# Kernel tuning notes

Hardware: AMD Instinct MI355X
Metric: run time of the kernel (lower is better)

## Reference

```python
import jax, jax.numpy as jnp
import numpy as np

B, FIN, H, W = 16, 256, 32, 32
NH, FH = 8, 64
CIN = FIN + 2  # fin + 2 coordinate-grid pos channels
COUT = NH * FH


def setup_inputs() -> dict:
    key = jax.random.key(0)
    ks = jax.random.split(key, 9)
    s = 1.0 / np.sqrt(CIN)
    so = 1.0 / np.sqrt(COUT)
    return {
        "x": jax.random.normal(ks[0], (B, FIN, H, W), dtype=jnp.float32),
        "wq": jax.random.uniform(ks[1], (COUT, CIN), jnp.float32, -s, s),
        "bq": jax.random.uniform(ks[2], (COUT,), jnp.float32, -s, s),
        "wk": jax.random.uniform(ks[3], (COUT, CIN), jnp.float32, -s, s),
        "bk": jax.random.uniform(ks[4], (COUT,), jnp.float32, -s, s),
        "wv": jax.random.uniform(ks[5], (COUT, CIN), jnp.float32, -s, s),
        "bv": jax.random.uniform(ks[6], (COUT,), jnp.float32, -s, s),
        "wo": jax.random.uniform(ks[7], (FIN, COUT), jnp.float32, -so, so),
        "bo": jax.random.uniform(ks[8], (FIN,), jnp.float32, -so, so),
    }


def reference(x, wq, bq, wk, bk, wv, bv, wo, bo):
    b, c, h, w = x.shape
    n = h * w
    # PosEncoding: concat one linspace(-1,1) coordinate channel per spatial dim
    gy, gx = jnp.meshgrid(jnp.linspace(-1.0, 1.0, h), jnp.linspace(-1.0, 1.0, w), indexing="ij")
    pos = jnp.broadcast_to(jnp.stack([gy, gx])[None], (b, 2, h, w)).astype(x.dtype)
    t = jnp.concatenate([x, pos], axis=1).reshape(b, c + 2, n)  # [B, C+2, N]
    # 1x1 convs are per-token GEMMs
    q = (jnp.einsum("oc,bcn->bon", wq, t) + bq[:, None]).reshape(b, NH, FH, n)
    k = (jnp.einsum("oc,bcn->bon", wk, t) + bk[:, None]).reshape(b, NH, FH, n)
    v = (jnp.einsum("oc,bcn->bon", wv, t) + bv[:, None]).reshape(b, NH, FH, n)
    temp = FH ** 0.5
    attn = jax.nn.softmax(jnp.einsum("bhdn,bhdm->bhnm", q, k) / temp, axis=-1)
    o = jnp.einsum("bhnm,bhdm->bhdn", attn, v).reshape(b, NH * FH, n)
    o = jnp.einsum("oc,bcn->bon", wo, o) + bo[:, None]
    return x + o.reshape(b, c, h, w)
```

## Files before the change

### kernel.cpp

```cpp
#include <hip/hip_runtime.h>


typedef unsigned short u16;
typedef unsigned int   u32;
typedef __attribute__((ext_vector_type(8))) short  short8;
typedef __attribute__((ext_vector_type(4))) float  float4_;

#define MFMA16(a, b, c) __builtin_amdgcn_mfma_f32_16x16x32_bf16(a, b, c, 0, 0, 0)

__device__ __forceinline__ float bf2f(u16 u) {
    union { u32 i; float f; } v; v.i = ((u32)u) << 16; return v.f;
}
__device__ __forceinline__ u16 f2bf(float f) {
    union { float f; u32 i; } v; v.f = f;
    u32 r = v.i + 0x7FFFu + ((v.i >> 16) & 1u);
    return (u16)(r >> 16);
}
__device__ __forceinline__ u16 f2bf_fast(float f) {
    union { float f; u32 i; } v; v.f = f;
    return (u16)((v.i + 0x8000u) >> 16);
}

__global__ __launch_bounds__(256) void prep(
    const float* __restrict__ wq, const float* __restrict__ wk,
    const float* __restrict__ wv, const float* __restrict__ x,
    u16* __restrict__ wb, u16* __restrict__ xT)
{
    __shared__ float Lt[64][65];
    const int bid = blockIdx.x;
    const int tid = threadIdx.x;
    if (bid < 512) {
        int i = bid * 256 + tid;
        int o = i >> 8, c = i & 255;
        size_t si = (size_t)o * 258 + c;
        wb[i]          = f2bf(wq[si]);
        wb[131072 + i] = f2bf(wk[si]);
        wb[262144 + i] = f2bf(wv[si]);
    } else {
        int r = bid - 512;
        int n0 = (r & 15) * 64, c0 = ((r >> 4) & 3) * 64, b = r >> 6;
#pragma unroll
        for (int p = 0; p < 4; ++p) {
            int c = p * 16 + (tid >> 4);
            int nn = (tid & 15) * 4;
            float4 v = *(const float4*)&x[((size_t)(b * 256) + c0 + c) * 1024 + n0 + nn];
            Lt[c][nn + 0] = v.x; Lt[c][nn + 1] = v.y;
            Lt[c][nn + 2] = v.z; Lt[c][nn + 3] = v.w;
        }
        __syncthreads();
#pragma unroll
        for (int p = 0; p < 4; ++p) {
            int n = p * 16 + (tid >> 4);
            int cc = (tid & 15) * 4;
            ushort4 st;
            st.x = f2bf(Lt[cc + 0][n]); st.y = f2bf(Lt[cc + 1][n]);
            st.z = f2bf(Lt[cc + 2][n]); st.w = f2bf(Lt[cc + 3][n]);
            *(ushort4*)&xT[((size_t)(b << 10) + n0 + n) * 256 + c0 + cc] = st;
        }
    }
}

__global__ __launch_bounds__(256) void qkv_mfma(
    const u16* __restrict__ xT, const u16* __restrict__ wb,
    const float* __restrict__ wq, const float* __restrict__ wk,
    const float* __restrict__ wv,
    const float* __restrict__ bq, const float* __restrict__ bk,
    const float* __restrict__ bv,
    u16* __restrict__ qkvbuf)
{
    __shared__ u16 Wl[128][40];
    __shared__ u16 Tl[128][40];
    const int tid = threadIdx.x;
    const int lane = tid & 63, w = tid >> 6;
    const int quad = lane >> 4, m15 = lane & 15;
    const int n0 = blockIdx.x * 128, mt = blockIdx.y, b = blockIdx.z;
    const int mat = mt >> 2;
    const int m0 = mt * 128;
    const float* worig = (mat == 0) ? wq : ((mat == 1) ? wk : wv);
    const float* bias  = (mat == 0) ? bq : ((mat == 1) ? bk : bv);
    const float oscale = (mat == 1) ? 0.125f : 1.0f;
    u16* outbuf = qkvbuf + (size_t)mat * 8388608;

    float4_ acc[2][8];
#pragma unroll
    for (int s = 0; s < 2; ++s)
#pragma unroll
        for (int t = 0; t < 8; ++t) acc[s][t] = (float4_){0, 0, 0, 0};

    const int row = tid >> 2, col8 = (tid & 3) * 8;

    for (int cc0 = 0; cc0 < 256; cc0 += 32) {
        __syncthreads();
#pragma unroll
        for (int rr = 0; rr < 128; rr += 64) {
            *(short8*)&Wl[row + rr][col8] =
                *(const short8*)(wb + (size_t)(m0 + row + rr) * 256 + cc0 + col8);
            *(short8*)&Tl[row + rr][col8] =
                *(const short8*)(xT + ((size_t)(b << 10) + n0 + row + rr) * 256 + cc0 + col8);
        }
        __syncthreads();
        short8 af[2];
#pragma unroll
        for (int s = 0; s < 2; ++s)
            af[s] = *(const short8*)&Wl[w * 32 + s * 16 + m15][quad * 8];
#pragma unroll
        for (int t = 0; t < 8; ++t) {
            short8 bf = *(const short8*)&Tl[t * 16 + m15][quad * 8];
#pragma unroll
            for (int s = 0; s < 2; ++s)
                acc[s][t] = MFMA16(af[s], bf, acc[s][t]);
        }
    }

#pragma unroll
    for (int s = 0; s < 2; ++s) {
        float wg[4], wx[4], bi[4];
#pragma unroll
        for (int r = 0; r < 4; ++r) {
            int om = (mt & 3) * 128 + w * 32 + s * 16 + quad * 4 + r;
            wg[r] = worig[(size_t)om * 258 + 256];
            wx[r] = worig[(size_t)om * 258 + 257];
            bi[r] = bias[om];
        }
        const int h = (mt & 3) * 2 + ((w * 32 + s * 16) >> 6);
        const int dbase = ((w * 32 + s * 16) & 63) + quad * 4;
#pragma unroll
        for (int t = 0; t < 8; ++t) {
            int n = n0 + t * 16 + m15;
            float gy = -1.0f + 2.0f * (float)(n >> 5) / 31.0f;
            float gx = -1.0f + 2.0f * (float)(n & 31) / 31.0f;
            float v[4];
#pragma unroll
            for (int r = 0; r < 4; ++r)
                v[r] = (acc[s][t][r] + wg[r] * gy + wx[r] * gx + bi[r]) * oscale;
            if (mat != 2) {
                ushort4 st;
                st.x = f2bf(v[0]); st.y = f2bf(v[1]);
                st.z = f2bf(v[2]); st.w = f2bf(v[3]);
                *(ushort4*)&outbuf[((size_t)(b * 8 + h) * 1024 + n) * 64 + dbase] = st;
            } else {
#pragma unroll
                for (int r = 0; r < 4; ++r)
                    outbuf[((size_t)(b * 8 + h) * 64 + dbase + r) * 1024 + n] = f2bf(v[r]);
            }
        }
    }
}

__global__ __launch_bounds__(256) void attn_mfma(
    u16* __restrict__ qbuf, const u16* __restrict__ kbuf,
    const u16* __restrict__ vbuf)
{
    __shared__ u16 Kl[64 * 64];
    __shared__ u16 Vl[64 * 64];
    __shared__ u16 Pl[4][32][72];

    const int tid = threadIdx.x;
    const int lane = tid & 63, w = tid >> 6;
    const int quad = lane >> 4, m15 = lane & 15;
    const int bh = blockIdx.x;
    const int q0 = blockIdx.y * 128;
    u16* qb = qbuf + (size_t)bh * 65536;
    const u16* kb = kbuf + (size_t)bh * 65536;
    const u16* vb = vbuf + (size_t)bh * 65536;

    short8 qf[2][2];
#pragma unroll
    for (int s = 0; s < 2; ++s) {
        const u16* qr = qb + (size_t)(q0 + w * 32 + s * 16 + m15) * 64 + quad * 8;
        qf[s][0] = *(const short8*)qr;
        qf[s][1] = *(const short8*)(qr + 32);
    }

    float4_ O[2][4];
    float lp[2][4];
#pragma unroll
    for (int s = 0; s < 2; ++s)
#pragma unroll
        for (int t = 0; t < 4; ++t) { O[s][t] = (float4_){0,0,0,0}; lp[s][t] = 0.0f; }

    const int row = tid >> 3, c8 = (tid & 7) * 8;
    const int stsw = c8 ^ ((row & 7) << 3);
    const int rdsw = (m15 & 7) << 3;

    for (int kt0 = 0; kt0 < 1024; kt0 += 64) {
        __syncthreads();
#pragma unroll
        for (int rr = 0; rr < 64; rr += 32) {
            *(short8*)&Kl[(row + rr) * 64 + stsw] =
                *(const short8*)(kb + (size_t)(kt0 + row + rr) * 64 + c8);
            *(short8*)&Vl[(row + rr) * 64 + stsw] =
                *(const short8*)(vb + (size_t)(row + rr) * 1024 + kt0 + c8);
        }
        __syncthreads();

        float4_ S[2][4];
#pragma unroll
        for (int s = 0; s < 2; ++s)
#pragma unroll
            for (int t = 0; t < 4; ++t) S[s][t] = (float4_){0, 0, 0, 0};
#pragma unroll
        for (int c = 0; c < 2; ++c) {
            short8 bk[4];
#pragma unroll
            for (int t = 0; t < 4; ++t)
                bk[t] = *(const short8*)&Kl[(t * 16 + m15) * 64 +
                                            ((c * 32 + quad * 8) ^ rdsw)];
            __builtin_amdgcn_s_setprio(1);
#pragma unroll
            for (int s = 0; s < 2; ++s)
#pragma unroll
                for (int t = 0; t < 4; ++t)
                    S[s][t] = MFMA16(qf[s][c], bk[t], S[s][t]);
            __builtin_amdgcn_s_setprio(0);
        }

#pragma unroll
        for (int s = 0; s < 2; ++s)
#pragma unroll
            for (int r = 0; r < 4; ++r) {
                float p0 = __expf(S[s][0][r]);
                float p1 = __expf(S[s][1][r]);
                float p2 = __expf(S[s][2][r]);
                float p3 = __expf(S[s][3][r]);
                u16* pr = &Pl[w][s * 16 + quad * 4 + r][m15];
                pr[0]  = f2bf_fast(p0);
                pr[16] = f2bf_fast(p1);
                pr[32] = f2bf_fast(p2);
                pr[48] = f2bf_fast(p3);
                lp[s][r] += (p0 + p1) + (p2 + p3);
            }

#pragma unroll
        for (int c = 0; c < 2; ++c) {
            short8 av[4];
#pragma unroll
            for (int dt = 0; dt < 4; ++dt)
                av[dt] = *(const short8*)&Vl[(dt * 16 + m15) * 64 +
                                             ((c * 32 + quad * 8) ^ rdsw)];
#pragma unroll
            for (int s = 0; s < 2; ++s) {
                short8 bp = *(const short8*)&Pl[w][s * 16 + m15][c * 32 + quad * 8];
                __builtin_amdgcn_s_setprio(1);
#pragma unroll
                for (int dt = 0; dt < 4; ++dt)
                    O[s][dt] = MFMA16(av[dt], bp, O[s][dt]);
                __builtin_amdgcn_s_setprio(0);
            }
        }
    }

#pragma unroll
    for (int s = 0; s < 2; ++s)
#pragma unroll
        for (int r = 0; r < 4; ++r) {
            float v = lp[s][r];
            v += __shfl_xor(v, 1);
            v += __shfl_xor(v, 2);
            v += __shfl_xor(v, 4);
            v += __shfl_xor(v, 8);
            lp[s][r] = v;
        }

#pragma unroll
    for (int s = 0; s < 2; ++s) {
        int src = (m15 >> 2) * 16;
        float a0 = __shfl(lp[s][0], src);
        float a1 = __shfl(lp[s][1], src);
        float a2 = __shfl(lp[s][2], src);
        float a3 = __shfl(lp[s][3], src);
        int rr2 = m15 & 3;
        float lq = (rr2 & 2) ? ((rr2 & 1) ? a3 : a2) : ((rr2 & 1) ? a1 : a0);
        float linv = 1.0f / lq;
        int n = q0 + w * 32 + s * 16 + m15;
#pragma unroll
        for (int dt = 0; dt < 4; ++dt) {
            ushort4 st;
            st.x = f2bf(O[s][dt][0] * linv);
            st.y = f2bf(O[s][dt][1] * linv);
            st.z = f2bf(O[s][dt][2] * linv);
            st.w = f2bf(O[s][dt][3] * linv);
            *(ushort4*)&qb[(size_t)n * 64 + dt * 16 + quad * 4] = st;
        }
    }
}

__global__ __launch_bounds__(256) void proj_mfma(
    const u16* __restrict__ ao, const float* __restrict__ wo,
    const float* __restrict__ bo, const float* __restrict__ x,
    float* __restrict__ out)
{
    __shared__ u16 Wl[64][72];
    __shared__ u16 Tl[64][72];
    const int tid = threadIdx.x;
    const int lane = tid & 63, w = tid >> 6;
    const int quad = lane >> 4, m15 = lane & 15;
    const int n0 = blockIdx.x * 64, f0 = blockIdx.y * 64, b = blockIdx.z;

    float4_ acc[4] = {{0,0,0,0},{0,0,0,0},{0,0,0,0},{0,0,0,0}};
    const int row = tid >> 3, c8 = (tid & 7) * 8;

    for (int cc0 = 0; cc0 < 512; cc0 += 64) {
        __syncthreads();
        const int h = cc0 >> 6;
#pragma unroll
        for (int rr = 0; rr < 64; rr += 32) {
            const float* wsrc = wo + (size_t)(f0 + row + rr) * 512 + cc0 + c8;
            float4 v0 = *(const float4*)wsrc;
            float4 v1 = *(const float4*)(wsrc + 4);
            ushort4 s0, s1;
            s0.x = f2bf(v0.x); s0.y = f2bf(v0.y); s0.z = f2bf(v0.z); s0.w = f2bf(v0.w);
            s1.x = f2bf(v1.x); s1.y = f2bf(v1.y); s1.z = f2bf(v1.z); s1.w = f2bf(v1.w);
            *(ushort4*)&Wl[row + rr][c8]     = s0;
            *(ushort4*)&Wl[row + rr][c8 + 4] = s1;
            *(short8*)&Tl[row + rr][c8] =
                *(const short8*)(ao + ((size_t)((b << 3) + h) * 1024 + n0 + row + rr) * 64 + c8);
        }
        __syncthreads();
#pragma unroll
        for (int c = 0; c < 2; ++c) {
            short8 af = *(const short8*)&Wl[w * 16 + m15][c * 32 + quad * 8];
#pragma unroll
            for (int t = 0; t < 4; ++t) {
                short8 bf = *(const short8*)&Tl[t * 16 + m15][c * 32 + quad * 8];
                acc[t] = MFMA16(af, bf, acc[t]);
            }
        }
    }

    float bi[4];
#pragma unroll
    for (int r = 0; r < 4; ++r) bi[r] = bo[f0 + w * 16 + quad * 4 + r];
#pragma unroll
    for (int t = 0; t < 4; ++t) {
        int n = n0 + t * 16 + m15;
#pragma unroll
        for (int r = 0; r < 4; ++r) {
            int f = f0 + w * 16 + quad * 4 + r;
            size_t idx = ((size_t)(b * 256) + f) * 1024 + n;
            out[idx] = acc[t][r] + bi[r] + x[idx];
        }
    }
}

extern "C" void kernel_launch(void* const* d_in, const int* in_sizes, int n_in,
                              void* d_out, int out_size, void* d_ws, size_t ws_size,
                              hipStream_t stream) {
    const float* x  = (const float*)d_in[0];
    const float* wq = (const float*)d_in[1];
    const float* bq = (const float*)d_in[2];
    const float* wk = (const float*)d_in[3];
    const float* bk = (const float*)d_in[4];
    const float* wv = (const float*)d_in[5];
    const float* bv = (const float*)d_in[6];
    const float* wo = (const float*)d_in[7];
    const float* bo = (const float*)d_in[8];

    u16* qkvbuf = (u16*)d_ws;
    u16* region = qkvbuf + 3 * 8388608;
    u16* xT = region;
    u16* wb = region + 4194304;

    prep<<<1536, 256, 0, stream>>>(wq, wk, wv, x, wb, xT);

    qkv_mfma<<<dim3(8, 12, 16), 256, 0, stream>>>(
        xT, wb, wq, wk, wv, bq, bk, bv, qkvbuf);

    attn_mfma<<<dim3(128, 8), 256, 0, stream>>>(
        qkvbuf, qkvbuf + 8388608, qkvbuf + 16777216);

    proj_mfma<<<dim3(16, 4, 16), 256, 0, stream>>>(qkvbuf, wo, bo, x, (float*)d_out);
}
```

Measured before the change: 202.0 us.

## Split attention work over 8 waves with 16 query rows each

```diff
diff --git a/kernel.cpp b/kernel.cpp
--- a/kernel.cpp
+++ b/kernel.cpp
@@ -147,13 +147,13 @@
     }
 }
 
-__global__ __launch_bounds__(256) void attn_mfma(
+__global__ __launch_bounds__(512, 8) void attn_mfma(
     u16* __restrict__ qbuf, const u16* __restrict__ kbuf,
     const u16* __restrict__ vbuf)
 {
     __shared__ u16 Kl[64 * 64];
     __shared__ u16 Vl[64 * 64];
-    __shared__ u16 Pl[4][32][72];
+    __shared__ u16 Pl[8][16][72];
 
     const int tid = threadIdx.x;
     const int lane = tid & 63, w = tid >> 6;
@@ -164,20 +164,17 @@
     const u16* kb = kbuf + (size_t)bh * 65536;
     const u16* vb = vbuf + (size_t)bh * 65536;
 
-    short8 qf[2][2];
-#pragma unroll
-    for (int s = 0; s < 2; ++s) {
-        const u16* qr = qb + (size_t)(q0 + w * 32 + s * 16 + m15) * 64 + quad * 8;
-        qf[s][0] = *(const short8*)qr;
-        qf[s][1] = *(const short8*)(qr + 32);
-    }
-
-    float4_ O[2][4];
-    float lp[2][4];
-#pragma unroll
-    for (int s = 0; s < 2; ++s)
-#pragma unroll
-        for (int t = 0; t < 4; ++t) { O[s][t] = (float4_){0,0,0,0}; lp[s][t] = 0.0f; }
+    short8 qf[2];
+    {
+        const u16* qr = qb + (size_t)(q0 + w * 16 + m15) * 64 + quad * 8;
+        qf[0] = *(const short8*)qr;
+        qf[1] = *(const short8*)(qr + 32);
+    }
+
+    float4_ O[4];
+    float lp[4];
+#pragma unroll
+    for (int t = 0; t < 4; ++t) { O[t] = (float4_){0,0,0,0}; lp[t] = 0.0f; }
 
     const int row = tid >> 3, c8 = (tid & 7) * 8;
     const int stsw = c8 ^ ((row & 7) << 3);
@@ -185,20 +182,15 @@
 
     for (int kt0 = 0; kt0 < 1024; kt0 += 64) {
         __syncthreads();
-#pragma unroll
-        for (int rr = 0; rr < 64; rr += 32) {
-            *(short8*)&Kl[(row + rr) * 64 + stsw] =
-                *(const short8*)(kb + (size_t)(kt0 + row + rr) * 64 + c8);
-            *(short8*)&Vl[(row + rr) * 64 + stsw] =
-                *(const short8*)(vb + (size_t)(row + rr) * 1024 + kt0 + c8);
-        }
-        __syncthreads();
-
-        float4_ S[2][4];
-#pragma unroll
-        for (int s = 0; s < 2; ++s)
-#pragma unroll
-            for (int t = 0; t < 4; ++t) S[s][t] = (float4_){0, 0, 0, 0};
+        *(short8*)&Kl[row * 64 + stsw] =
+            *(const short8*)(kb + (size_t)(kt0 + row) * 64 + c8);
+        *(short8*)&Vl[row * 64 + stsw] =
+            *(const short8*)(vb + (size_t)row * 1024 + kt0 + c8);
+        __syncthreads();
+
+        float4_ S[4];
+#pragma unroll
+        for (int t = 0; t < 4; ++t) S[t] = (float4_){0, 0, 0, 0};
 #pragma unroll
         for (int c = 0; c < 2; ++c) {
             short8 bk[4];
@@ -208,78 +200,68 @@
                                             ((c * 32 + quad * 8) ^ rdsw)];
             __builtin_amdgcn_s_setprio(1);
 #pragma unroll
-            for (int s = 0; s < 2; ++s)
-#pragma unroll
-                for (int t = 0; t < 4; ++t)
-                    S[s][t] = MFMA16(qf[s][c], bk[t], S[s][t]);
+            for (int t = 0; t < 4; ++t)
+                S[t] = MFMA16(qf[c], bk[t], S[t]);
             __builtin_amdgcn_s_setprio(0);
         }
 
 #pragma unroll
-        for (int s = 0; s < 2; ++s)
-#pragma unroll
-            for (int r = 0; r < 4; ++r) {
-                float p0 = __expf(S[s][0][r]);
-                float p1 = __expf(S[s][1][r]);
-                float p2 = __expf(S[s][2][r]);
-                float p3 = __expf(S[s][3][r]);
-                u16* pr = &Pl[w][s * 16 + quad * 4 + r][m15];
-                pr[0]  = f2bf_fast(p0);
-                pr[16] = f2bf_fast(p1);
-                pr[32] = f2bf_fast(p2);
-                pr[48] = f2bf_fast(p3);
-                lp[s][r] += (p0 + p1) + (p2 + p3);
-            }
+        for (int r = 0; r < 4; ++r) {
+            float p0 = __expf(S[0][r]);
+            float p1 = __expf(S[1][r]);
+            float p2 = __expf(S[2][r]);
+            float p3 = __expf(S[3][r]);
+            u16* pr = &Pl[w][quad * 4 + r][m15];
+            pr[0]  = f2bf_fast(p0);
+            pr[16] = f2bf_fast(p1);
+            pr[32] = f2bf_fast(p2);
+            pr[48] = f2bf_fast(p3);
+            lp[r] += (p0 + p1) + (p2 + p3);
+        }
 
 #pragma unroll
         for (int c = 0; c < 2; ++c) {
+            short8 bp = *(const short8*)&Pl[w][m15][c * 32 + quad * 8];
             short8 av[4];
 #pragma unroll
             for (int dt = 0; dt < 4; ++dt)
                 av[dt] = *(const short8*)&Vl[(dt * 16 + m15) * 64 +
                                              ((c * 32 + quad * 8) ^ rdsw)];
-#pragma unroll
-            for (int s = 0; s < 2; ++s) {
-                short8 bp = *(const short8*)&Pl[w][s * 16 + m15][c * 32 + quad * 8];
-                __builtin_amdgcn_s_setprio(1);
-#pragma unroll
-                for (int dt = 0; dt < 4; ++dt)
-                    O[s][dt] = MFMA16(av[dt], bp, O[s][dt]);
-                __builtin_amdgcn_s_setprio(0);
-            }
-        }
-    }
-
-#pragma unroll
-    for (int s = 0; s < 2; ++s)
-#pragma unroll
-        for (int r = 0; r < 4; ++r) {
-            float v = lp[s][r];
-            v += __shfl_xor(v, 1);
-            v += __shfl_xor(v, 2);
-            v += __shfl_xor(v, 4);
-            v += __shfl_xor(v, 8);
-            lp[s][r] = v;
-        }
-
-#pragma unroll
-    for (int s = 0; s < 2; ++s) {
+            __builtin_amdgcn_s_setprio(1);
+#pragma unroll
+            for (int dt = 0; dt < 4; ++dt)
+                O[dt] = MFMA16(av[dt], bp, O[dt]);
+            __builtin_amdgcn_s_setprio(0);
+        }
+    }
+
+#pragma unroll
+    for (int r = 0; r < 4; ++r) {
+        float v = lp[r];
+        v += __shfl_xor(v, 1);
+        v += __shfl_xor(v, 2);
+        v += __shfl_xor(v, 4);
+        v += __shfl_xor(v, 8);
+        lp[r] = v;
+    }
+
+    {
         int src = (m15 >> 2) * 16;
-        float a0 = __shfl(lp[s][0], src);
-        float a1 = __shfl(lp[s][1], src);
-        float a2 = __shfl(lp[s][2], src);
-        float a3 = __shfl(lp[s][3], src);
+        float a0 = __shfl(lp[0], src);
+        float a1 = __shfl(lp[1], src);
+        float a2 = __shfl(lp[2], src);
+        float a3 = __shfl(lp[3], src);
         int rr2 = m15 & 3;
         float lq = (rr2 & 2) ? ((rr2 & 1) ? a3 : a2) : ((rr2 & 1) ? a1 : a0);
         float linv = 1.0f / lq;
-        int n = q0 + w * 32 + s * 16 + m15;
+        int n = q0 + w * 16 + m15;
 #pragma unroll
         for (int dt = 0; dt < 4; ++dt) {
             ushort4 st;
-            st.x = f2bf(O[s][dt][0] * linv);
-            st.y = f2bf(O[s][dt][1] * linv);
-            st.z = f2bf(O[s][dt][2] * linv);
-            st.w = f2bf(O[s][dt][3] * linv);
+            st.x = f2bf(O[dt][0] * linv);
+            st.y = f2bf(O[dt][1] * linv);
+            st.z = f2bf(O[dt][2] * linv);
+            st.w = f2bf(O[dt][3] * linv);
             *(ushort4*)&qb[(size_t)n * 64 + dt * 16 + quad * 4] = st;
         }
     }
@@ -366,7 +348,7 @@
     qkv_mfma<<<dim3(8, 12, 16), 256, 0, stream>>>(
         xT, wb, wq, wk, wv, bq, bk, bv, qkvbuf);
 
-    attn_mfma<<<dim3(128, 8), 256, 0, stream>>>(
+    attn_mfma<<<dim3(128, 8), 512, 0, stream>>>(
         qkvbuf, qkvbuf + 8388608, qkvbuf + 16777216);
 
     proj_mfma<<<dim3(16, 4, 16), 256, 0, stream>>>(qkvbuf, wo, bo, x, (float*)d_out);
```

Result: slower. 232.7 us (+15.2%).

## Transpose QK^T MFMA so each lane owns a query row, packing P stores

Applied to the files above, without the earlier changes.

```diff
diff --git a/kernel.cpp b/kernel.cpp
--- a/kernel.cpp
+++ b/kernel.cpp
@@ -15,10 +15,6 @@
     union { float f; u32 i; } v; v.f = f;
     u32 r = v.i + 0x7FFFu + ((v.i >> 16) & 1u);
     return (u16)(r >> 16);
-}
-__device__ __forceinline__ u16 f2bf_fast(float f) {
-    union { float f; u32 i; } v; v.f = f;
-    return (u16)((v.i + 0x8000u) >> 16);
 }
 
 __global__ __launch_bounds__(256) void prep(
@@ -153,7 +149,7 @@
 {
     __shared__ u16 Kl[64 * 64];
     __shared__ u16 Vl[64 * 64];
-    __shared__ u16 Pl[4][32][72];
+    __shared__ u16 Pl[4][2][16][72];
 
     const int tid = threadIdx.x;
     const int lane = tid & 63, w = tid >> 6;
@@ -173,15 +169,16 @@
     }
 
     float4_ O[2][4];
-    float lp[2][4];
+    float lp[2] = {0.0f, 0.0f};
 #pragma unroll
     for (int s = 0; s < 2; ++s)
 #pragma unroll
-        for (int t = 0; t < 4; ++t) { O[s][t] = (float4_){0,0,0,0}; lp[s][t] = 0.0f; }
+        for (int t = 0; t < 4; ++t) O[s][t] = (float4_){0,0,0,0};
 
     const int row = tid >> 3, c8 = (tid & 7) * 8;
     const int stsw = c8 ^ ((row & 7) << 3);
     const int rdsw = (m15 & 7) << 3;
+    const int psw  = (m15 & 3) << 3;
 
     for (int kt0 = 0; kt0 < 1024; kt0 += 64) {
         __syncthreads();
@@ -201,35 +198,39 @@
             for (int t = 0; t < 4; ++t) S[s][t] = (float4_){0, 0, 0, 0};
 #pragma unroll
         for (int c = 0; c < 2; ++c) {
-            short8 bk[4];
+            short8 kf[4];
 #pragma unroll
             for (int t = 0; t < 4; ++t)
-                bk[t] = *(const short8*)&Kl[(t * 16 + m15) * 64 +
+                kf[t] = *(const short8*)&Kl[(t * 16 + m15) * 64 +
                                             ((c * 32 + quad * 8) ^ rdsw)];
             __builtin_amdgcn_s_setprio(1);
 #pragma unroll
             for (int s = 0; s < 2; ++s)
 #pragma unroll
                 for (int t = 0; t < 4; ++t)
-                    S[s][t] = MFMA16(qf[s][c], bk[t], S[s][t]);
+                    S[s][t] = MFMA16(kf[t], qf[s][c], S[s][t]);
             __builtin_amdgcn_s_setprio(0);
         }
 
 #pragma unroll
-        for (int s = 0; s < 2; ++s)
-#pragma unroll
-            for (int r = 0; r < 4; ++r) {
-                float p0 = __expf(S[s][0][r]);
-                float p1 = __expf(S[s][1][r]);
-                float p2 = __expf(S[s][2][r]);
-                float p3 = __expf(S[s][3][r]);
-                u16* pr = &Pl[w][s * 16 + quad * 4 + r][m15];
-                pr[0]  = f2bf_fast(p0);
-                pr[16] = f2bf_fast(p1);
-                pr[32] = f2bf_fast(p2);
-                pr[48] = f2bf_fast(p3);
-                lp[s][r] += (p0 + p1) + (p2 + p3);
+        for (int s = 0; s < 2; ++s) {
+            float lsum = 0.0f;
+#pragma unroll
+            for (int t = 0; t < 4; ++t) {
+                float p0 = __expf(S[s][t][0]);
+                float p1 = __expf(S[s][t][1]);
+                float p2 = __expf(S[s][t][2]);
+                float p3 = __expf(S[s][t][3]);
+                u32 w0, w1;
+                asm("v_cvt_pk_bf16_f32 %0, %1, %2" : "=v"(w0) : "v"(p0), "v"(p1));
+                asm("v_cvt_pk_bf16_f32 %0, %1, %2" : "=v"(w1) : "v"(p2), "v"(p3));
+                const int col = (t * 16 + quad * 4) ^ psw;
+                uint2 st; st.x = w0; st.y = w1;
+                *(uint2*)&Pl[w][s][m15][col] = st;
+                lsum += (p0 + p1) + (p2 + p3);
             }
+            lp[s] += lsum;
+        }
 
 #pragma unroll
         for (int c = 0; c < 2; ++c) {
@@ -240,7 +241,7 @@
                                              ((c * 32 + quad * 8) ^ rdsw)];
 #pragma unroll
             for (int s = 0; s < 2; ++s) {
-                short8 bp = *(const short8*)&Pl[w][s * 16 + m15][c * 32 + quad * 8];
+                short8 bp = *(const short8*)&Pl[w][s][m15][(c * 32 + quad * 8) ^ psw];
                 __builtin_amdgcn_s_setprio(1);
 #pragma unroll
                 for (int dt = 0; dt < 4; ++dt)
@@ -251,27 +252,11 @@
     }
 
 #pragma unroll
-    for (int s = 0; s < 2; ++s)
-#pragma unroll
-        for (int r = 0; r < 4; ++r) {
-            float v = lp[s][r];
-            v += __shfl_xor(v, 1);
-            v += __shfl_xor(v, 2);
-            v += __shfl_xor(v, 4);
-            v += __shfl_xor(v, 8);
-            lp[s][r] = v;
-        }
-
-#pragma unroll
     for (int s = 0; s < 2; ++s) {
-        int src = (m15 >> 2) * 16;
-        float a0 = __shfl(lp[s][0], src);
-        float a1 = __shfl(lp[s][1], src);
-        float a2 = __shfl(lp[s][2], src);
-        float a3 = __shfl(lp[s][3], src);
-        int rr2 = m15 & 3;
-        float lq = (rr2 & 2) ? ((rr2 & 1) ? a3 : a2) : ((rr2 & 1) ? a1 : a0);
-        float linv = 1.0f / lq;
+        float v = lp[s];
+        v += __shfl_xor(v, 16);
+        v += __shfl_xor(v, 32);
+        float linv = 1.0f / v;
         int n = q0 + w * 32 + s * 16 + m15;
 #pragma unroll
         for (int dt = 0; dt < 4; ++dt) {
```

New measurement: 199.3 us. Within noise of the previous version (-1.3%).
